# Performance work log

Hardware: AMD Instinct MI355X
Metric: run time of the kernel (lower is better)

## Reference

```python
import jax, jax.numpy as jnp
import numpy as np

N = 100_000      # nodes
E = 2_500_000    # edges (nnz), avg degree 25
D_IN = 32
D_OUT = 32


def setup_inputs() -> dict:
    key = jax.random.key(0)
    k1, k2, k3, k4 = jax.random.split(key, 4)
    X = jax.random.normal(k1, (N, D_IN), dtype=jnp.float32)
    # CSR row offsets: sorted, anchored at 0 and E
    rp = jnp.sort(jax.random.randint(k2, (N + 1,), 0, E, dtype=jnp.int32))
    rp = rp.at[0].set(0).at[-1].set(E)
    ci = jax.random.randint(k3, (E,), 0, N, dtype=jnp.int32)
    W = (jax.random.normal(k4, (D_IN, D_OUT), dtype=jnp.float32)
         * (1.0 / np.sqrt(D_OUT)).astype(np.float32))
    dummy = jnp.zeros((1,), dtype=jnp.int32)
    return {
        "X": X,
        "weights": W,
        "row_pointers": rp,
        "column_index": ci,
        "blockPartition": dummy,
        "edgeToColumn": dummy,
        "edgeToRow": dummy,
        "hybrid_type": dummy,
        "row_nzr": dummy,
        "col_nzr": dummy,
    }


def reference(X, weights, row_pointers, column_index, blockPartition,
              edgeToColumn, edgeToRow, hybrid_type, row_nzr, col_nzr):
    # Fused GIN: X_prime = A @ X (CSR neighbor sum), then X_prime @ W.
    # Recover per-edge destination row from CSR offsets: row r owns edges
    # in [row_pointers[r], row_pointers[r+1]).
    edge_ids = jnp.arange(E, dtype=row_pointers.dtype)
    row = jnp.searchsorted(row_pointers, edge_ids, side="right") - 1  # [E]
    gathered = X[column_index]                       # [E, D_IN] (irregular gather)
    X_prime = jax.ops.segment_sum(gathered, row, num_segments=N)  # [N, D_IN]
    return X_prime @ weights                          # [N, D_OUT]
```

## Files before the change

kernel.cpp:

```cpp
#include <hip/hip_runtime.h>

#define D 32

__global__ __launch_bounds__(256, 4)
void gin_fused(const float* __restrict__ X,
               const float* __restrict__ W,
               const int* __restrict__ rp,
               const int* __restrict__ ci,
               float* __restrict__ out,
               int n) {
    __shared__ float Wl[D * D];

    int tid = threadIdx.x;
    {
        const float4* Wv = (const float4*)W;
        float4* Wlv = (float4*)Wl;
        Wlv[tid] = Wv[tid];
    }
    __syncthreads();

    int wave = tid >> 6;
    int lane = tid & 63;
    int row = blockIdx.x * 4 + wave;
    if (row >= n) return;

    int start = rp[row];
    int end   = rp[row + 1];

    int g = lane >> 3;
    int s = lane & 7;

    float4 acc = make_float4(0.f, 0.f, 0.f, 0.f);
    for (int e = start + g; e < end; e += 8) {
        int c = ci[e];
        const float4 xr = ((const float4*)(X + (size_t)c * D))[s];
        acc.x += xr.x; acc.y += xr.y; acc.z += xr.z; acc.w += xr.w;
    }

    #pragma unroll
    for (int off = 8; off < 64; off <<= 1) {
        acc.x += __shfl_xor(acc.x, off, 64);
        acc.y += __shfl_xor(acc.y, off, 64);
        acc.z += __shfl_xor(acc.z, off, 64);
        acc.w += __shfl_xor(acc.w, off, 64);
    }

    int j = lane & 31;
    float o = 0.f;
    #pragma unroll
    for (int sg = 0; sg < 8; ++sg) {
        float ax = __shfl(acc.x, sg, 64);
        float ay = __shfl(acc.y, sg, 64);
        float az = __shfl(acc.z, sg, 64);
        float aw = __shfl(acc.w, sg, 64);
        int d = 4 * sg;
        o += ax * Wl[(d    ) * D + j];
        o += ay * Wl[(d + 1) * D + j];
        o += az * Wl[(d + 2) * D + j];
        o += aw * Wl[(d + 3) * D + j];
    }
    if (lane < 32) out[(size_t)row * D + j] = o;
}

extern "C" void kernel_launch(void* const* d_in, const int* in_sizes, int n_in,
                              void* d_out, int out_size, void* d_ws, size_t ws_size,
                              hipStream_t stream) {
    const float* X  = (const float*)d_in[0];
    const float* W  = (const float*)d_in[1];
    const int*   rp = (const int*)d_in[2];
    const int*   ci = (const int*)d_in[3];
    float* out = (float*)d_out;

    int n = in_sizes[2] - 1;
    int blocks = (n + 3) / 4;
    hipLaunchKernelGGL(gin_fused, dim3(blocks), dim3(256), 0, stream,
                       X, W, rp, ci, out, n);
}
```

Measured before the change: 161.3 us.

## Process two rows per wave with batched index loads and unrolled gathers

Each wave now handles two adjacent rows. It loads the row pointers once and reads up to 64 column indices per row with a single coalesced load, then broadcasts them by shuffle. The X gathers for both rows are unrolled into register arrays so many loads are in flight before accumulation, which raises memory-level parallelism over the old dependent index-then-load loop. The cost is higher register pressure from 16 float4 buffers, masked padding work when the two rows' degrees differ, and half as many waves.

```diff
diff --git a/kernel.cpp b/kernel.cpp
--- a/kernel.cpp
+++ b/kernel.cpp
@@ -3,63 +3,122 @@
 #define D 32
 
 __global__ __launch_bounds__(256, 4)
-void gin_fused(const float* __restrict__ X,
-               const float* __restrict__ W,
-               const int* __restrict__ rp,
-               const int* __restrict__ ci,
-               float* __restrict__ out,
-               int n) {
+void gin_fused2(const float* __restrict__ X,
+                const float* __restrict__ W,
+                const int* __restrict__ rp,
+                const int* __restrict__ ci,
+                float* __restrict__ out,
+                int n) {
     __shared__ float Wl[D * D];
-
     int tid = threadIdx.x;
-    {
-        const float4* Wv = (const float4*)W;
-        float4* Wlv = (float4*)Wl;
-        Wlv[tid] = Wv[tid];
-    }
+    ((float4*)Wl)[tid] = ((const float4*)W)[tid];
     __syncthreads();
 
-    int wave = tid >> 6;
-    int lane = tid & 63;
-    int row = blockIdx.x * 4 + wave;
-    if (row >= n) return;
+    int wave = tid >> 6, lane = tid & 63;
+    int r0 = (blockIdx.x * 4 + wave) * 2;
+    if (r0 >= n) return;
+    bool haveB = (r0 + 1 < n);
 
-    int start = rp[row];
-    int end   = rp[row + 1];
+    int nrp = haveB ? 3 : 2;
+    int rv = (lane < nrp) ? rp[r0 + lane] : 0;
+    int e0 = __shfl(rv, 0, 64);
+    int e1 = __shfl(rv, 1, 64);
+    int e2 = haveB ? __shfl(rv, 2, 64) : e1;
+
+    int startA = e0, degA = e1 - e0;
+    int startB = e1, degB = e2 - e1;
 
     int g = lane >> 3;
     int s = lane & 7;
 
-    float4 acc = make_float4(0.f, 0.f, 0.f, 0.f);
-    for (int e = start + g; e < end; e += 8) {
-        int c = ci[e];
-        const float4 xr = ((const float4*)(X + (size_t)c * D))[s];
-        acc.x += xr.x; acc.y += xr.y; acc.z += xr.z; acc.w += xr.w;
+    float4 accA = make_float4(0.f, 0.f, 0.f, 0.f);
+    float4 accB = make_float4(0.f, 0.f, 0.f, 0.f);
+
+    int degM = degA > degB ? degA : degB;
+    for (int cb = 0; cb < degM; cb += 64) {
+        int remA = degA - cb, remB = degB - cb;
+
+        int ciA = 0, ciB = 0;
+        if (remA > 0) {
+            int li = cb + lane; li = li < degA ? li : degA - 1;
+            ciA = ci[startA + li];
+        }
+        if (remB > 0) {
+            int li = cb + lane; li = li < degB ? li : degB - 1;
+            ciB = ci[startB + li];
+        }
+
+        float4 xA[8], xB[8];
+        #pragma unroll
+        for (int it = 0; it < 8; ++it) {
+            if (it * 8 < remA) {
+                int l = it * 8 + g;
+                int c = __shfl(ciA, l < remA ? l : remA - 1, 64);
+                xA[it] = ((const float4*)(X + (size_t)c * D))[s];
+            }
+        }
+        #pragma unroll
+        for (int it = 0; it < 8; ++it) {
+            if (it * 8 < remB) {
+                int l = it * 8 + g;
+                int c = __shfl(ciB, l < remB ? l : remB - 1, 64);
+                xB[it] = ((const float4*)(X + (size_t)c * D))[s];
+            }
+        }
+        #pragma unroll
+        for (int it = 0; it < 8; ++it) {
+            if (it * 8 < remA) {
+                float m = (it * 8 + g < remA) ? 1.f : 0.f;
+                accA.x = fmaf(m, xA[it].x, accA.x);
+                accA.y = fmaf(m, xA[it].y, accA.y);
+                accA.z = fmaf(m, xA[it].z, accA.z);
+                accA.w = fmaf(m, xA[it].w, accA.w);
+            }
+        }
+        #pragma unroll
+        for (int it = 0; it < 8; ++it) {
+            if (it * 8 < remB) {
+                float m = (it * 8 + g < remB) ? 1.f : 0.f;
+                accB.x = fmaf(m, xB[it].x, accB.x);
+                accB.y = fmaf(m, xB[it].y, accB.y);
+                accB.z = fmaf(m, xB[it].z, accB.z);
+                accB.w = fmaf(m, xB[it].w, accB.w);
+            }
+        }
     }
 
     #pragma unroll
     for (int off = 8; off < 64; off <<= 1) {
-        acc.x += __shfl_xor(acc.x, off, 64);
-        acc.y += __shfl_xor(acc.y, off, 64);
-        acc.z += __shfl_xor(acc.z, off, 64);
-        acc.w += __shfl_xor(acc.w, off, 64);
+        accA.x += __shfl_xor(accA.x, off, 64);
+        accA.y += __shfl_xor(accA.y, off, 64);
+        accA.z += __shfl_xor(accA.z, off, 64);
+        accA.w += __shfl_xor(accA.w, off, 64);
+        accB.x += __shfl_xor(accB.x, off, 64);
+        accB.y += __shfl_xor(accB.y, off, 64);
+        accB.z += __shfl_xor(accB.z, off, 64);
+        accB.w += __shfl_xor(accB.w, off, 64);
     }
 
     int j = lane & 31;
-    float o = 0.f;
+    float oA = 0.f, oB = 0.f;
     #pragma unroll
     for (int sg = 0; sg < 8; ++sg) {
-        float ax = __shfl(acc.x, sg, 64);
-        float ay = __shfl(acc.y, sg, 64);
-        float az = __shfl(acc.z, sg, 64);
-        float aw = __shfl(acc.w, sg, 64);
         int d = 4 * sg;
-        o += ax * Wl[(d    ) * D + j];
-        o += ay * Wl[(d + 1) * D + j];
-        o += az * Wl[(d + 2) * D + j];
-        o += aw * Wl[(d + 3) * D + j];
+        float a;
+        a = __shfl(accA.x, sg, 64); oA = fmaf(a, Wl[(d    ) * D + j], oA);
+        a = __shfl(accA.y, sg, 64); oA = fmaf(a, Wl[(d + 1) * D + j], oA);
+        a = __shfl(accA.z, sg, 64); oA = fmaf(a, Wl[(d + 2) * D + j], oA);
+        a = __shfl(accA.w, sg, 64); oA = fmaf(a, Wl[(d + 3) * D + j], oA);
+        a = __shfl(accB.x, sg, 64); oB = fmaf(a, Wl[(d    ) * D + j], oB);
+        a = __shfl(accB.y, sg, 64); oB = fmaf(a, Wl[(d + 1) * D + j], oB);
+        a = __shfl(accB.z, sg, 64); oB = fmaf(a, Wl[(d + 2) * D + j], oB);
+        a = __shfl(accB.w, sg, 64); oB = fmaf(a, Wl[(d + 3) * D + j], oB);
     }
-    if (lane < 32) out[(size_t)row * D + j] = o;
+    if (lane < 32) {
+        out[(size_t)r0 * D + j] = oA;
+    } else if (haveB) {
+        out[(size_t)(r0 + 1) * D + j] = oB;
+    }
 }
 
 extern "C" void kernel_launch(void* const* d_in, const int* in_sizes, int n_in,
@@ -72,7 +131,8 @@
     float* out = (float*)d_out;
 
     int n = in_sizes[2] - 1;
-    int blocks = (n + 3) / 4;
-    hipLaunchKernelGGL(gin_fused, dim3(blocks), dim3(256), 0, stream,
+    int pairs = (n + 1) / 2;
+    int blocks = (pairs + 3) / 4;
+    hipLaunchKernelGGL(gin_fused2, dim3(blocks), dim3(256), 0, stream,
                        X, W, rp, ci, out, n);
 }
```

After: 169.3 us. 1.05x slower.
